# Kernel optimization log

Measured on AMD Instinct MI355X. Metric: run time of the kernel, lower is better.

The kernel has to match this reference:

```python
import jax, jax.numpy as jnp
import numpy as np

DIM = 1024
HEADS = 16
D_K = DIM // HEADS


def setup_inputs() -> dict:
    key = jax.random.key(0)
    k1, k2, k3, k4 = jax.random.split(key, 4)
    s = 1.0 / np.sqrt(DIM)
    return {
        "x": jax.random.normal(k1, (8, 1024, DIM), dtype=jnp.float32),
        "w_qkv": jax.random.uniform(k2, (DIM, 3 * DIM), dtype=jnp.float32, minval=-s, maxval=s),
        "w_out": jax.random.uniform(k3, (DIM, DIM), dtype=jnp.float32, minval=-s, maxval=s),
        "b_out": jax.random.uniform(k4, (DIM,), dtype=jnp.float32, minval=-s, maxval=s),
    }


def reference(x, w_qkv, w_out, b_out):
    B, N, _ = x.shape
    scale = D_K ** -0.5
    qkv = x @ w_qkv                                   # [B, N, 3*dim]
    q, k, v = jnp.split(qkv, 3, axis=-1)
    # [B, N, dim] -> [B, H, N, d_k]
    def heads(t):
        return t.reshape(B, N, HEADS, D_K).transpose(0, 2, 1, 3)
    q, k, v = heads(q), heads(k), heads(v)
    dots = jnp.einsum("bhnd,bhmd->bhnm", q, k) * scale  # [B, H, N, N]
    attn = jax.nn.softmax(dots, axis=-1)
    out = jnp.einsum("bhnm,bhmd->bhnd", attn, v)        # [B, H, N, d_k]
    out = out.transpose(0, 2, 1, 3).reshape(B, N, HEADS * D_K)
    return out @ w_out + b_out
```

## Files before the change

kernel.cpp:

```cpp
#include <hip/hip_runtime.h>
#include <hip/hip_bf16.h>
#include <math.h>


typedef __attribute__((ext_vector_type(8))) _Float16 f16x8;
typedef __attribute__((ext_vector_type(4))) _Float16 f16x4;
typedef __attribute__((ext_vector_type(4))) float f32x4;
typedef __attribute__((ext_vector_type(16))) float f32x16;
typedef __attribute__((ext_vector_type(4))) unsigned int u32x4;

#define QK_SCALE 0.18033688011112042f

#define GLOBAL_LOAD_LDS16(g, l) \
  __builtin_amdgcn_global_load_lds((const __attribute__((address_space(1))) void*)(g), \
                                   (__attribute__((address_space(3))) void*)(l), 16, 0, 0)

__global__ __launch_bounds__(256) void cast_all(
    const float* __restrict__ x, _Float16* __restrict__ xh,
    const float* __restrict__ w_qkv, _Float16* __restrict__ wqT,
    const float* __restrict__ w_out, _Float16* __restrict__ woT) {
  __shared__ _Float16 hs[64][65];
  const int blk = blockIdx.x;
  const int t = threadIdx.x;

  if (blk < 2048) {
    const int n4 = 8192 * 1024 / 4;
    int i = blk * 256 + t;
    const int stride = 2048 * 256;
    for (; i < n4; i += stride) {
      float4 v = ((const float4*)x)[i];
      f16x4 h;
      h[0] = (_Float16)v.x; h[1] = (_Float16)v.y;
      h[2] = (_Float16)v.z; h[3] = (_Float16)v.w;
      ((f16x4*)xh)[i] = h;
    }
    return;
  }

  const float* in;
  _Float16* hi;
  int R, C, bx, by;
  if (blk < 2048 + 768) {
    const int id = blk - 2048;
    in = w_qkv; hi = wqT; R = 1024; C = 3072;
    bx = id % 48; by = id / 48;
  } else {
    const int id = blk - 2816;
    in = w_out; hi = woT; R = 1024; C = 1024;
    bx = id % 16; by = id / 16;
  }
  const int r0 = by * 64, c0 = bx * 64;
#pragma unroll
  for (int it = 0; it < 4; ++it) {
    int r = (t >> 4) + it * 16;
    int cc = (t & 15) * 4;
    float4 v = *(const float4*)(in + (size_t)(r0 + r) * C + c0 + cc);
    hs[r][cc + 0] = (_Float16)v.x;
    hs[r][cc + 1] = (_Float16)v.y;
    hs[r][cc + 2] = (_Float16)v.z;
    hs[r][cc + 3] = (_Float16)v.w;
  }
  __syncthreads();
  const int oc = t >> 2;
  const int rr = (t & 3) * 16;
#pragma unroll
  for (int g = 0; g < 2; ++g) {
    f16x8 a;
#pragma unroll
    for (int j = 0; j < 8; ++j) a[j] = hs[rr + g * 8 + j][oc];
    *(f16x8*)(hi + (size_t)(c0 + oc) * R + r0 + rr + g * 8) = a;
  }
}

__global__ __launch_bounds__(256) void gemm1_qkv(
    const _Float16* __restrict__ Ah, const _Float16* __restrict__ Bh,
    _Float16* __restrict__ qkout, _Float16* __restrict__ vTout) {
  __shared__ char lds[34816];
  const int K = 1024;
  const int tid = threadIdx.x;
  const int wave = tid >> 6, lane = tid & 63;
  const int m0 = blockIdx.y * 128, n0 = blockIdx.x * 128;
  const int wr = wave >> 1, wc = wave & 1;

  const int srow_off = lane >> 3;
  const int slot     = lane & 7;

  const int lr = lane & 15, kg = lane >> 4;

  f32x4 acc[4][4];
#pragma unroll
  for (int m = 0; m < 4; ++m)
#pragma unroll
    for (int n = 0; n < 4; ++n) acc[m][n] = (f32x4){0.f, 0.f, 0.f, 0.f};

  const _Float16* gbase[2];
  gbase[0] = Ah + (size_t)m0 * K;
  gbase[1] = Bh + (size_t)n0 * K;

  for (int k0 = 0; k0 < K; k0 += 64) {
    __syncthreads();
#pragma unroll
    for (int p = 0; p < 2; ++p) {
#pragma unroll
      for (int it = 0; it < 4; ++it) {
        const int rbase = wave * 32 + it * 8;
        const int r  = rbase + srow_off;
        const int gc = slot ^ (r & 7);
        const _Float16* g = gbase[p] + (size_t)r * K + k0 + gc * 8;
        GLOBAL_LOAD_LDS16(g, lds + p * 16384 + rbase * 128);
      }
    }
    __syncthreads();

#pragma unroll
    for (int s2 = 0; s2 < 2; ++s2) {
      f16x8 af[4], bf[4];
      const int c = s2 * 4 + kg;
#pragma unroll
      for (int m = 0; m < 4; ++m) {
        const int e = wr * 64 + m * 16 + lr;
        af[m] = *(const f16x8*)(lds + 0 * 16384 + e * 128 + ((c ^ (e & 7)) * 16));
      }
#pragma unroll
      for (int n = 0; n < 4; ++n) {
        const int e = wc * 64 + n * 16 + lr;
        bf[n] = *(const f16x8*)(lds + 1 * 16384 + e * 128 + ((c ^ (e & 7)) * 16));
      }
#pragma unroll
      for (int m = 0; m < 4; ++m)
#pragma unroll
        for (int n = 0; n < 4; ++n)
          acc[m][n] = __builtin_amdgcn_mfma_f32_16x16x32_f16(af[m], bf[n], acc[m][n], 0, 0, 0);
    }
  }

  const int crow = (lane >> 4) * 4, ccol = lane & 15;
  if (n0 < 2048) {
    const float qsc = (n0 < 1024) ? (float)QK_SCALE : 1.0f;
#pragma unroll
    for (int m = 0; m < 4; ++m) {
#pragma unroll
      for (int n = 0; n < 4; ++n) {
        const int rbase = m0 + wr * 64 + m * 16 + crow;
        const int cc = n0 + wc * 64 + n * 16 + ccol;
#pragma unroll
        for (int i = 0; i < 4; ++i)
          qkout[(size_t)(rbase + i) * 2048 + cc] = (_Float16)(acc[m][n][i] * qsc);
      }
    }
  } else {
    __syncthreads();
    _Float16* lv = (_Float16*)lds;
#pragma unroll
    for (int m = 0; m < 4; ++m)
#pragma unroll
      for (int n = 0; n < 4; ++n) {
        const int cc = wc * 64 + n * 16 + ccol;
#pragma unroll
        for (int i = 0; i < 4; ++i) {
          const int r = wr * 64 + m * 16 + crow + i;
          lv[cc * 136 + r] = (_Float16)acc[m][n][i];
        }
      }
    __syncthreads();
    const int bb = m0 >> 10, seq0 = m0 & 1023;
    const int hbase = (n0 - 2048) >> 6;
#pragma unroll
    for (int it = 0; it < 8; ++it) {
      const int idx = tid + it * 256;
      const int cc = idx >> 4, ch = idx & 15;
      f16x8 v = *(const f16x8*)(lv + cc * 136 + ch * 8);
      const int hh = hbase + (cc >> 6), d = cc & 63;
      *(f16x8*)(vTout + (((size_t)bb * 16 + hh) * 64 + d) * 1024 + seq0 + ch * 8) = v;
    }
  }
}

__global__ __launch_bounds__(256) void attn_mfma(
    const _Float16* __restrict__ qk,
    const _Float16* __restrict__ vT,
    _Float16* __restrict__ ao) {
  const int hb   = blockIdx.x;
  const int h    = hb >> 3;
  const int b    = hb & 7;
  const int band = blockIdx.y;
  const int tid  = threadIdx.x;
  const int wave = tid >> 6;
  const int lane = tid & 63;
  const int l31  = lane & 31;
  const int hi   = lane >> 5;
  const int kswz = (l31 & 7) << 4;

  __shared__ _Float16 Ks[2][64 * 64];
  __shared__ _Float16 Vt[2][64 * 64];

  const _Float16* vbase = vT + ((size_t)(b * 16 + h) * 64) * 1024;

  const int qrow_g = b * 1024 + band * 128 + wave * 32 + l31;
  f16x8 qf[4];
#pragma unroll
  for (int c = 0; c < 4; ++c)
    qf[c] = *(const f16x8*)(qk + (size_t)qrow_g * 2048 + h * 64 + c * 16 + hi * 8);

  f16x8 vones;
#pragma unroll
  for (int j = 0; j < 8; ++j) vones[j] = (_Float16)1.0f;

  f32x16 accO0 = {0}, accO1 = {0}, accL = {0};

  const int srow8 = (lane >> 3);
  const int slot  = lane & 7;

  auto stage_t = [&](int t, int buf) {
#pragma unroll
    for (int it = 0; it < 2; ++it) {
      const int r  = wave * 8 + srow8 + it * 32;
      const int gc = slot ^ (r & 7);
      const _Float16* gk = qk + (size_t)(b * 1024 + t * 64 + r) * 2048 +
                           1024 + h * 64 + gc * 8;
      const _Float16* gv = vbase + (size_t)r * 1024 + t * 64 + gc * 8;
      char* dk = (char*)&Ks[buf][0] + (wave * 8 + it * 32) * 128;
      char* dv = (char*)&Vt[buf][0] + (wave * 8 + it * 32) * 128;
      GLOBAL_LOAD_LDS16(gk, dk);
      GLOBAL_LOAD_LDS16(gv, dv);
    }
  };

  stage_t(0, 0);

  for (int t = 0; t < 16; ++t) {
    __syncthreads();
    if (t < 15) stage_t(t + 1, (t + 1) & 1);
    const int buf = t & 1;
    const char* ksb = (const char*)&Ks[buf][0];
    const char* vtb = (const char*)&Vt[buf][0];

    f32x16 accS0 = {0}, accS1 = {0};
    __builtin_amdgcn_s_setprio(1);
#pragma unroll
    for (int c = 0; c < 4; ++c) {
      f16x8 ka0 = *(const f16x8*)(ksb + l31 * 128 + ((c * 32 + hi * 16) ^ kswz));
      f16x8 ka1 = *(const f16x8*)(ksb + (l31 + 32) * 128 + ((c * 32 + hi * 16) ^ kswz));
      accS0 = __builtin_amdgcn_mfma_f32_32x32x16_f16(ka0, qf[c], accS0, 0, 0, 0);
      accS1 = __builtin_amdgcn_mfma_f32_32x32x16_f16(ka1, qf[c], accS1, 0, 0, 0);
    }
    __builtin_amdgcn_s_setprio(0);

#pragma unroll
    for (int c = 0; c < 4; ++c) {
      float e[8];
#pragma unroll
      for (int k = 0; k < 8; ++k)
        e[k] = __builtin_exp2f((c < 2) ? accS0[(c & 1) * 8 + k]
                                       : accS1[(c & 1) * 8 + k]);
      unsigned q0a = __builtin_bit_cast(unsigned, __builtin_amdgcn_cvt_pkrtz(e[0], e[1]));
      unsigned q0b = __builtin_bit_cast(unsigned, __builtin_amdgcn_cvt_pkrtz(e[2], e[3]));
      unsigned q1a = __builtin_bit_cast(unsigned, __builtin_amdgcn_cvt_pkrtz(e[4], e[5]));
      unsigned q1b = __builtin_bit_cast(unsigned, __builtin_amdgcn_cvt_pkrtz(e[6], e[7]));
      unsigned send_a = hi ? q0a : q1a;
      unsigned send_b = hi ? q0b : q1b;
      unsigned recv_a = __shfl_xor(send_a, 32);
      unsigned recv_b = __shfl_xor(send_b, 32);
      u32x4 pu;
      pu[0] = hi ? recv_a : q0a;
      pu[1] = hi ? recv_b : q0b;
      pu[2] = hi ? q1a : recv_a;
      pu[3] = hi ? q1b : recv_b;
      f16x8 pa = __builtin_bit_cast(f16x8, pu);

      const int kchunk = ((2 * c + hi) * 16) ^ kswz;
      f16x8 vb0 = *(const f16x8*)(vtb + l31 * 128 + kchunk);
      f16x8 vb1 = *(const f16x8*)(vtb + (l31 + 32) * 128 + kchunk);
      __builtin_amdgcn_s_setprio(1);
      accO0 = __builtin_amdgcn_mfma_f32_32x32x16_f16(pa, vb0, accO0, 0, 0, 0);
      accO1 = __builtin_amdgcn_mfma_f32_32x32x16_f16(pa, vb1, accO1, 0, 0, 0);
      accL  = __builtin_amdgcn_mfma_f32_32x32x16_f16(pa, vones, accL, 0, 0, 0);
      __builtin_amdgcn_s_setprio(0);
    }
  }

#pragma unroll
  for (int reg = 0; reg < 16; ++reg) {
    const int qr = (reg & 3) + 8 * (reg >> 2) + 4 * hi;
    const float il = 1.f / accL[reg];
    const size_t grow = (size_t)(b * 1024 + band * 128 + wave * 32 + qr) * 1024 + h * 64;
    ao[grow + l31]      = (_Float16)(accO0[reg] * il);
    ao[grow + 32 + l31] = (_Float16)(accO1[reg] * il);
  }
}

__global__ __launch_bounds__(256) void gemm2_out(
    const _Float16* __restrict__ A,
    const _Float16* __restrict__ B,
    float* __restrict__ C, const float* __restrict__ bias) {
  __shared__ char lds[2 * 8192];
  const int K = 1024;
  const int tid = threadIdx.x;
  const int wave = tid >> 6, lane = tid & 63;
  const int m0 = blockIdx.y * 128, n0 = blockIdx.x * 128;
  const int wr = wave >> 1, wc = wave & 1;

  const int srow = lane >> 2;
  const int sgchunk = (lane & 3) ^ ((srow >> 1) & 3);
  const int lr = lane & 15, kg = lane >> 4;
  const int rdoff = lr * 64 + ((kg ^ ((lr >> 1) & 3)) * 16);

  f32x4 acc[4][4];
#pragma unroll
  for (int m = 0; m < 4; ++m)
#pragma unroll
    for (int n = 0; n < 4; ++n) acc[m][n] = (f32x4){0.f, 0.f, 0.f, 0.f};

  const _Float16* gbase[2];
  gbase[0] = A + (size_t)m0 * K;
  gbase[1] = B + (size_t)n0 * K;

  for (int k0 = 0; k0 < K; k0 += 32) {
    __syncthreads();
#pragma unroll
    for (int p = 0; p < 2; ++p) {
#pragma unroll
      for (int half = 0; half < 2; ++half) {
        const int r16 = wave * 32 + half * 16;
        const _Float16* g = gbase[p] + (size_t)(r16 + srow) * K + k0 + sgchunk * 8;
        GLOBAL_LOAD_LDS16(g, lds + p * 8192 + r16 * 64);
      }
    }
    __syncthreads();

    f16x8 af[4], bf[4];
#pragma unroll
    for (int m = 0; m < 4; ++m)
      af[m] = *(const f16x8*)(lds + 0 * 8192 + (wr * 64 + m * 16) * 64 + rdoff);
#pragma unroll
    for (int n = 0; n < 4; ++n)
      bf[n] = *(const f16x8*)(lds + 1 * 8192 + (wc * 64 + n * 16) * 64 + rdoff);
#pragma unroll
    for (int m = 0; m < 4; ++m)
#pragma unroll
      for (int n = 0; n < 4; ++n)
        acc[m][n] = __builtin_amdgcn_mfma_f32_16x16x32_f16(af[m], bf[n], acc[m][n], 0, 0, 0);
  }

  const int crow = (lane >> 4) * 4, ccol = lane & 15;
#pragma unroll
  for (int m = 0; m < 4; ++m) {
#pragma unroll
    for (int n = 0; n < 4; ++n) {
      const int rbase = m0 + wr * 64 + m * 16 + crow;
      const int c = n0 + wc * 64 + n * 16 + ccol;
      const float bv = bias[c];
#pragma unroll
      for (int i = 0; i < 4; ++i)
        C[(size_t)(rbase + i) * 1024 + c] = acc[m][n][i] + bv;
    }
  }
}

extern "C" void kernel_launch(void* const* d_in, const int* in_sizes, int n_in,
                              void* d_out, int out_size, void* d_ws, size_t ws_size,
                              hipStream_t stream) {
  const float* x     = (const float*)d_in[0];
  const float* w_qkv = (const float*)d_in[1];
  const float* w_out = (const float*)d_in[2];
  const float* b_out = (const float*)d_in[3];
  float* out = (float*)d_out;

  char* ws = (char*)d_ws;
  _Float16* xh  = (_Float16*)(ws);
  _Float16* ao  = xh;
  _Float16* wqT = (_Float16*)(ws + (32u << 20));
  _Float16* woT = (_Float16*)(ws + (44u << 20));
  _Float16* qkp = (_Float16*)(ws + (48u << 20));
  _Float16* vT  = (_Float16*)(ws + (80u << 20));

  cast_all<<<3072, 256, 0, stream>>>(x, xh, w_qkv, wqT, w_out, woT);

  gemm1_qkv<<<dim3(24, 64), 256, 0, stream>>>(xh, wqT, qkp, vT);

  attn_mfma<<<dim3(128, 8), 256, 0, stream>>>(qkp, vT, ao);

  gemm2_out<<<dim3(8, 64), 256, 0, stream>>>(ao, woT, out, b_out);
}
```

Baseline: 176.5 us.

## Use 8-wave attention blocks over 256 rows and 64-wide K tiles in output GEMM

```diff
diff --git a/kernel.cpp b/kernel.cpp
--- a/kernel.cpp
+++ b/kernel.cpp
@@ -84,7 +84,6 @@
 
   const int srow_off = lane >> 3;
   const int slot     = lane & 7;
-
   const int lr = lane & 15, kg = lane >> 4;
 
   f32x4 acc[4][4];
@@ -176,7 +175,7 @@
   }
 }
 
-__global__ __launch_bounds__(256) void attn_mfma(
+__global__ __launch_bounds__(512) void attn_mfma(
     const _Float16* __restrict__ qk,
     const _Float16* __restrict__ vT,
     _Float16* __restrict__ ao) {
@@ -196,11 +195,11 @@
 
   const _Float16* vbase = vT + ((size_t)(b * 16 + h) * 64) * 1024;
 
-  const int qrow_g = b * 1024 + band * 128 + wave * 32 + l31;
+  const int row0 = b * 1024 + band * 256 + wave * 32;
   f16x8 qf[4];
 #pragma unroll
   for (int c = 0; c < 4; ++c)
-    qf[c] = *(const f16x8*)(qk + (size_t)qrow_g * 2048 + h * 64 + c * 16 + hi * 8);
+    qf[c] = *(const f16x8*)(qk + (size_t)(row0 + l31) * 2048 + h * 64 + c * 16 + hi * 8);
 
   f16x8 vones;
 #pragma unroll
@@ -208,22 +207,19 @@
 
   f32x16 accO0 = {0}, accO1 = {0}, accL = {0};
 
-  const int srow8 = (lane >> 3);
+  const int srow8 = lane >> 3;
   const int slot  = lane & 7;
+  const int gc    = slot ^ srow8;
 
   auto stage_t = [&](int t, int buf) {
-#pragma unroll
-    for (int it = 0; it < 2; ++it) {
-      const int r  = wave * 8 + srow8 + it * 32;
-      const int gc = slot ^ (r & 7);
-      const _Float16* gk = qk + (size_t)(b * 1024 + t * 64 + r) * 2048 +
-                           1024 + h * 64 + gc * 8;
-      const _Float16* gv = vbase + (size_t)r * 1024 + t * 64 + gc * 8;
-      char* dk = (char*)&Ks[buf][0] + (wave * 8 + it * 32) * 128;
-      char* dv = (char*)&Vt[buf][0] + (wave * 8 + it * 32) * 128;
-      GLOBAL_LOAD_LDS16(gk, dk);
-      GLOBAL_LOAD_LDS16(gv, dv);
-    }
+    const int r = wave * 8 + srow8;
+    const _Float16* gk = qk + (size_t)(b * 1024 + t * 64 + r) * 2048 +
+                         1024 + h * 64 + gc * 8;
+    const _Float16* gv = vbase + (size_t)r * 1024 + t * 64 + gc * 8;
+    char* dk = (char*)&Ks[buf][0] + wave * 8 * 128;
+    char* dv = (char*)&Vt[buf][0] + wave * 8 * 128;
+    GLOBAL_LOAD_LDS16(gk, dk);
+    GLOBAL_LOAD_LDS16(gv, dv);
   };
 
   stage_t(0, 0);
@@ -283,7 +279,7 @@
   for (int reg = 0; reg < 16; ++reg) {
     const int qr = (reg & 3) + 8 * (reg >> 2) + 4 * hi;
     const float il = 1.f / accL[reg];
-    const size_t grow = (size_t)(b * 1024 + band * 128 + wave * 32 + qr) * 1024 + h * 64;
+    const size_t grow = (size_t)(row0 + qr) * 1024 + h * 64;
     ao[grow + l31]      = (_Float16)(accO0[reg] * il);
     ao[grow + 32 + l31] = (_Float16)(accO1[reg] * il);
   }
@@ -293,17 +289,16 @@
     const _Float16* __restrict__ A,
     const _Float16* __restrict__ B,
     float* __restrict__ C, const float* __restrict__ bias) {
-  __shared__ char lds[2 * 8192];
+  __shared__ char lds[2 * 16384];
   const int K = 1024;
   const int tid = threadIdx.x;
   const int wave = tid >> 6, lane = tid & 63;
   const int m0 = blockIdx.y * 128, n0 = blockIdx.x * 128;
   const int wr = wave >> 1, wc = wave & 1;
 
-  const int srow = lane >> 2;
-  const int sgchunk = (lane & 3) ^ ((srow >> 1) & 3);
+  const int srow_off = lane >> 3;
+  const int slot     = lane & 7;
   const int lr = lane & 15, kg = lane >> 4;
-  const int rdoff = lr * 64 + ((kg ^ ((lr >> 1) & 3)) * 16);
 
   f32x4 acc[4][4];
 #pragma unroll
@@ -315,31 +310,41 @@
   gbase[0] = A + (size_t)m0 * K;
   gbase[1] = B + (size_t)n0 * K;
 
-  for (int k0 = 0; k0 < K; k0 += 32) {
+  for (int k0 = 0; k0 < K; k0 += 64) {
     __syncthreads();
 #pragma unroll
     for (int p = 0; p < 2; ++p) {
 #pragma unroll
-      for (int half = 0; half < 2; ++half) {
-        const int r16 = wave * 32 + half * 16;
-        const _Float16* g = gbase[p] + (size_t)(r16 + srow) * K + k0 + sgchunk * 8;
-        GLOBAL_LOAD_LDS16(g, lds + p * 8192 + r16 * 64);
-      }
-    }
-    __syncthreads();
-
-    f16x8 af[4], bf[4];
-#pragma unroll
-    for (int m = 0; m < 4; ++m)
-      af[m] = *(const f16x8*)(lds + 0 * 8192 + (wr * 64 + m * 16) * 64 + rdoff);
-#pragma unroll
-    for (int n = 0; n < 4; ++n)
-      bf[n] = *(const f16x8*)(lds + 1 * 8192 + (wc * 64 + n * 16) * 64 + rdoff);
-#pragma unroll
-    for (int m = 0; m < 4; ++m)
-#pragma unroll
-      for (int n = 0; n < 4; ++n)
-        acc[m][n] = __builtin_amdgcn_mfma_f32_16x16x32_f16(af[m], bf[n], acc[m][n], 0, 0, 0);
+      for (int it = 0; it < 4; ++it) {
+        const int rbase = wave * 32 + it * 8;
+        const int r  = rbase + srow_off;
+        const int gc = slot ^ (r & 7);
+        const _Float16* g = gbase[p] + (size_t)r * K + k0 + gc * 8;
+        GLOBAL_LOAD_LDS16(g, lds + p * 16384 + rbase * 128);
+      }
+    }
+    __syncthreads();
+
+#pragma unroll
+    for (int s2 = 0; s2 < 2; ++s2) {
+      f16x8 af[4], bf[4];
+      const int c = s2 * 4 + kg;
+#pragma unroll
+      for (int m = 0; m < 4; ++m) {
+        const int e = wr * 64 + m * 16 + lr;
+        af[m] = *(const f16x8*)(lds + 0 * 16384 + e * 128 + ((c ^ (e & 7)) * 16));
+      }
+#pragma unroll
+      for (int n = 0; n < 4; ++n) {
+        const int e = wc * 64 + n * 16 + lr;
+        bf[n] = *(const f16x8*)(lds + 1 * 16384 + e * 128 + ((c ^ (e & 7)) * 16));
+      }
+#pragma unroll
+      for (int m = 0; m < 4; ++m)
+#pragma unroll
+        for (int n = 0; n < 4; ++n)
+          acc[m][n] = __builtin_amdgcn_mfma_f32_16x16x32_f16(af[m], bf[n], acc[m][n], 0, 0, 0);
+    }
   }
 
   const int crow = (lane >> 4) * 4, ccol = lane & 15;
@@ -378,7 +383,7 @@
 
   gemm1_qkv<<<dim3(24, 64), 256, 0, stream>>>(xh, wqT, qkp, vT);
 
-  attn_mfma<<<dim3(128, 8), 256, 0, stream>>>(qkp, vT, ao);
+  attn_mfma<<<dim3(128, 4), 512, 0, stream>>>(qkp, vT, ao);
 
   gemm2_out<<<dim3(8, 64), 256, 0, stream>>>(ao, woT, out, b_out);
 }
```

New measurement: 178.4 us. No clear change (+1.1%).
